# Kernel optimization log

Hardware: AMD Instinct MI355X
Metric: run time of the kernel (lower is better)

Reference implementation:

```python
import jax, jax.numpy as jnp
import numpy as np

B, S, D, H = 4, 2048, 1024, 16
DK = D // H


def setup_inputs() -> dict:
    key = jax.random.key(0)
    ks = jax.random.split(key, 12)
    inp = {
        'q': jax.random.normal(ks[0], (B, S, D), jnp.float32),
        'k': jax.random.normal(ks[1], (B, S, D), jnp.float32),
        'v': jax.random.normal(ks[2], (B, S, D), jnp.float32),
        # causal mask, broadcast over batch and heads
        'mask': jnp.tril(jnp.ones((S, S), jnp.int32))[None, None, :, :],
        'wq_w': jax.random.normal(ks[3], (D, D), jnp.float32) / np.sqrt(D),
        'wq_b': jax.random.normal(ks[4], (D,), jnp.float32) * 0.01,
        'wk_w': jax.random.normal(ks[5], (D, D), jnp.float32) / np.sqrt(D),
        'wk_b': jax.random.normal(ks[6], (D,), jnp.float32) * 0.01,
        'wv_w': jax.random.normal(ks[7], (D, D), jnp.float32) / np.sqrt(D),
        'wv_b': jax.random.normal(ks[8], (D,), jnp.float32) * 0.01,
        'wo_w': jax.random.normal(ks[9], (D, D), jnp.float32) / np.sqrt(D),
        'wo_b': jax.random.normal(ks[10], (D,), jnp.float32) * 0.01,
    }
    return inp


def reference(q, k, v, mask, wq_w, wq_b, wk_w, wk_b, wv_w, wv_b, wo_w, wo_b):
    # torch Linear: y = x @ W.T + b
    def split_heads(x):
        b, s, _ = x.shape
        return x.reshape(b, s, H, DK).transpose(0, 2, 1, 3)  # [B,H,S,DK]

    query = split_heads(q @ wq_w.T + wq_b)
    key_ = split_heads(k @ wk_w.T + wk_b)
    value = split_heads(v @ wv_w.T + wv_b)

    scores = jnp.einsum('bhqd,bhkd->bhqk', query, key_) / jnp.sqrt(
        jnp.asarray(DK, query.dtype))
    scores = jnp.where(mask == 0, jnp.asarray(-1e9, scores.dtype), scores)
    attn = jax.nn.softmax(scores, axis=-1)  # dropout=0.0 (eval)
    x = jnp.einsum('bhqk,bhkd->bhqd', attn, value)
    x = x.transpose(0, 2, 1, 3).reshape(q.shape[0], q.shape[1], D)
    out = x @ wo_w.T + wo_b
    return (out, attn)
```

## Files before the change

kernel.cpp:

```cpp
#include <hip/hip_runtime.h>
#include <stdint.h>

typedef unsigned short u16;
typedef short short8 __attribute__((ext_vector_type(8)));
typedef float f32x4 __attribute__((ext_vector_type(4)));

#define NB 4
#define NS 2048
#define ND 1024
#define NH 16
#define NDK 64

__device__ __forceinline__ u16 f2bf(float f) {
    union { float f; uint32_t i; } x; x.f = f;
    uint32_t r = x.i + 0x7FFFu + ((x.i >> 16) & 1u);
    return (u16)(r >> 16);
}
__device__ __forceinline__ float bf2f(u16 u) {
    union { uint32_t i; float f; } x; x.i = ((uint32_t)u) << 16; return x.f;
}
__device__ __forceinline__ short8 cvt8(const float* __restrict__ p) {
    float4 a = *(const float4*)p;
    float4 b = *(const float4*)(p + 4);
    short8 r;
    r[0] = (short)f2bf(a.x); r[1] = (short)f2bf(a.y);
    r[2] = (short)f2bf(a.z); r[3] = (short)f2bf(a.w);
    r[4] = (short)f2bf(b.x); r[5] = (short)f2bf(b.y);
    r[6] = (short)f2bf(b.z); r[7] = (short)f2bf(b.w);
    return r;
}

template<int MODE>
__global__ __launch_bounds__(256) void gemm128(
    const void* __restrict__ Av, const float* __restrict__ Bt,
    const float* __restrict__ bias, void* __restrict__ Cv)
{
    __shared__ __align__(16) u16 As[128 * 40];
    __shared__ __align__(16) u16 Bs[128 * 40];
    const int tid  = threadIdx.x;
    const int lane = tid & 63;
    const int w    = tid >> 6;
    const int wm   = (w >> 1) * 64;
    const int wn   = (w & 1) * 64;
    const int l15  = lane & 15;
    const int quad = lane >> 4;
    const int K    = 1024;
    int mt, nt;
    if (MODE == 2) { mt = blockIdx.x & 7; nt = blockIdx.x >> 3; }
    else           { mt = blockIdx.x >> 3; nt = blockIdx.x & 7; }
    const int m0 = mt * 128, n0 = nt * 128;

    f32x4 acc[4][4];
    const f32x4 zf = {0.f, 0.f, 0.f, 0.f};
#pragma unroll
    for (int i = 0; i < 4; ++i)
#pragma unroll
        for (int j = 0; j < 4; ++j) acc[i][j] = zf;

    const int r0 = tid >> 2;
    const int c0 = (tid & 3) * 8;

    const float* Af = (const float*)Av;
    const u16*   Ab = (const u16*)Av;
    const float* Bp = Bt + (size_t)(n0 + r0) * K + c0;

    for (int k0 = 0; k0 < K; k0 += 32) {
        __syncthreads();
        short8 a0, a1;
        if (MODE == 3) {
            a0 = *(const short8*)(Ab + (size_t)(m0 + r0) * K + c0 + k0);
            a1 = *(const short8*)(Ab + (size_t)(m0 + r0 + 64) * K + c0 + k0);
        } else {
            a0 = cvt8(Af + (size_t)(m0 + r0) * K + c0 + k0);
            a1 = cvt8(Af + (size_t)(m0 + r0 + 64) * K + c0 + k0);
        }
        short8 b0 = cvt8(Bp + k0);
        short8 b1 = cvt8(Bp + k0 + (size_t)64 * K);
        *(short8*)(As + r0 * 40 + c0)        = a0;
        *(short8*)(As + (r0 + 64) * 40 + c0) = a1;
        *(short8*)(Bs + r0 * 40 + c0)        = b0;
        *(short8*)(Bs + (r0 + 64) * 40 + c0) = b1;
        __syncthreads();
        short8 af[4], bfr[4];
#pragma unroll
        for (int i = 0; i < 4; ++i)
            af[i] = *(const short8*)(As + (wm + i * 16 + l15) * 40 + quad * 8);
#pragma unroll
        for (int j = 0; j < 4; ++j)
            bfr[j] = *(const short8*)(Bs + (wn + j * 16 + l15) * 40 + quad * 8);
#pragma unroll
        for (int i = 0; i < 4; ++i)
#pragma unroll
            for (int j = 0; j < 4; ++j)
                acc[i][j] = __builtin_amdgcn_mfma_f32_16x16x32_bf16(af[i], bfr[j], acc[i][j], 0, 0, 0);
    }

    if (MODE != 2) {
#pragma unroll
        for (int j = 0; j < 4; ++j) {
            const int n = n0 + wn + j * 16 + l15;
            const float bv = bias[n];
#pragma unroll
            for (int i = 0; i < 4; ++i) {
#pragma unroll
                for (int r = 0; r < 4; ++r) {
                    const int m = m0 + wm + i * 16 + quad * 4 + r;
                    const float vv = acc[i][j][r] + bv;
                    if (MODE == 3) {
                        ((float*)Cv)[(size_t)m * ND + n] = vv;
                    } else {
                        const size_t idx = ((size_t)((m >> 11) * NH + (n >> 6)) << 17)
                                         + (size_t)(m & (NS - 1)) * NDK + (n & (NDK - 1));
                        ((u16*)Cv)[idx] = f2bf(vv);
                    }
                }
            }
        }
    } else {
#pragma unroll
        for (int i = 0; i < 4; ++i) {
#pragma unroll
            for (int r = 0; r < 4; ++r) {
                const int m = m0 + wm + i * 16 + quad * 4 + r;
                const float bv = bias[m];
#pragma unroll
                for (int j = 0; j < 4; ++j) {
                    const int n = n0 + wn + j * 16 + l15;
                    const float vv = acc[i][j][r] + bv;
                    const size_t idx = ((size_t)((n >> 11) * NH + (m >> 6)) << 17)
                                     + (size_t)(m & (NDK - 1)) * NS + (n & (NS - 1));
                    ((u16*)Cv)[idx] = f2bf(vv);
                }
            }
        }
    }
}

__global__ __launch_bounds__(256) void attn64(
    const u16* __restrict__ Qh, const u16* __restrict__ Kh,
    const u16* __restrict__ Vt, float* __restrict__ attn,
    u16* __restrict__ X)
{
    __shared__ __align__(16) u16 Qs[64 * 72];
    __shared__ __align__(16) u16 Ks[64 * 72];
    __shared__ __align__(16) u16 Vs[64 * 72];
    __shared__ __align__(16) u16 Ps[64 * 72];
    const int tid  = threadIdx.x;
    const int lane = tid & 63;
    const int w    = tid >> 6;
    const int l15  = lane & 15;
    const int quad = lane >> 4;
    const int q0 = blockIdx.x * 64;
    const int bh = blockIdx.y;
    const u16* Qp = Qh + ((size_t)bh * NS + q0) * NDK;
    const u16* Kp = Kh + (size_t)bh * NS * NDK;
    const u16* Vp = Vt + (size_t)bh * NDK * NS;

    const int lr = tid >> 3;
    const int lc = (tid & 7) * 8;

    *(uint4*)(Qs + lr * 72 + lc)        = *(const uint4*)(Qp + (size_t)lr * NDK + lc);
    *(uint4*)(Qs + (lr + 32) * 72 + lc) = *(const uint4*)(Qp + (size_t)(lr + 32) * NDK + lc);
    __syncthreads();

    const int qrow = q0 + w * 16 + quad * 4;

    float m_r[4], l_r[4];
#pragma unroll
    for (int r = 0; r < 4; ++r) { m_r[r] = -1e30f; l_r[r] = 0.f; }

    const int nkt = (q0 >> 6) + 1;

    for (int kt = 0; kt < nkt; ++kt) {
        const int k0 = kt * 64;
        __syncthreads();
        *(uint4*)(Ks + lr * 72 + lc)        = *(const uint4*)(Kp + (size_t)(k0 + lr) * NDK + lc);
        *(uint4*)(Ks + (lr + 32) * 72 + lc) = *(const uint4*)(Kp + (size_t)(k0 + lr + 32) * NDK + lc);
        __syncthreads();

        f32x4 sa[4];
        const f32x4 zf = {0.f, 0.f, 0.f, 0.f};
#pragma unroll
        for (int j = 0; j < 4; ++j) sa[j] = zf;
#pragma unroll
        for (int ks = 0; ks < 64; ks += 32) {
            const short8 a = *(const short8*)(Qs + (w * 16 + l15) * 72 + ks + quad * 8);
#pragma unroll
            for (int j = 0; j < 4; ++j) {
                const short8 b = *(const short8*)(Ks + (j * 16 + l15) * 72 + ks + quad * 8);
                sa[j] = __builtin_amdgcn_mfma_f32_16x16x32_bf16(a, b, sa[j], 0, 0, 0);
            }
        }
        float s[4][4];
#pragma unroll
        for (int j = 0; j < 4; ++j) {
            const int kg = k0 + j * 16 + l15;
#pragma unroll
            for (int r = 0; r < 4; ++r)
                s[j][r] = (kg > qrow + r) ? -1e9f : sa[j][r] * 0.125f;
        }
#pragma unroll
        for (int r = 0; r < 4; ++r) {
            float mx = fmaxf(fmaxf(s[0][r], s[1][r]), fmaxf(s[2][r], s[3][r]));
            mx = fmaxf(mx, __shfl_xor(mx, 1));
            mx = fmaxf(mx, __shfl_xor(mx, 2));
            mx = fmaxf(mx, __shfl_xor(mx, 4));
            mx = fmaxf(mx, __shfl_xor(mx, 8));
            const float mn = fmaxf(m_r[r], mx);
            float sum = __expf(s[0][r] - mn) + __expf(s[1][r] - mn)
                      + __expf(s[2][r] - mn) + __expf(s[3][r] - mn);
            sum += __shfl_xor(sum, 1);
            sum += __shfl_xor(sum, 2);
            sum += __shfl_xor(sum, 4);
            sum += __shfl_xor(sum, 8);
            l_r[r] = l_r[r] * __expf(m_r[r] - mn) + sum;
            m_r[r] = mn;
        }
    }

    float rl[4];
#pragma unroll
    for (int r = 0; r < 4; ++r) rl[r] = 1.f / l_r[r];

    f32x4 oa[4];
    {
        const f32x4 zf = {0.f, 0.f, 0.f, 0.f};
#pragma unroll
        for (int j = 0; j < 4; ++j) oa[j] = zf;
    }

    float* arow = attn + (size_t)bh * NS * NS;

    for (int kt = 0; kt < NS / 64; ++kt) {
        const int k0 = kt * 64;
        if (k0 < q0 + 64) {
            __syncthreads();
            *(uint4*)(Ks + lr * 72 + lc)        = *(const uint4*)(Kp + (size_t)(k0 + lr) * NDK + lc);
            *(uint4*)(Ks + (lr + 32) * 72 + lc) = *(const uint4*)(Kp + (size_t)(k0 + lr + 32) * NDK + lc);
            *(uint4*)(Vs + lr * 72 + lc)        = *(const uint4*)(Vp + (size_t)lr * NS + k0 + lc);
            *(uint4*)(Vs + (lr + 32) * 72 + lc) = *(const uint4*)(Vp + (size_t)(lr + 32) * NS + k0 + lc);
            __syncthreads();

            f32x4 sa[4];
            const f32x4 zf = {0.f, 0.f, 0.f, 0.f};
#pragma unroll
            for (int j = 0; j < 4; ++j) sa[j] = zf;
#pragma unroll
            for (int ks = 0; ks < 64; ks += 32) {
                const short8 a = *(const short8*)(Qs + (w * 16 + l15) * 72 + ks + quad * 8);
#pragma unroll
                for (int j = 0; j < 4; ++j) {
                    const short8 b = *(const short8*)(Ks + (j * 16 + l15) * 72 + ks + quad * 8);
                    sa[j] = __builtin_amdgcn_mfma_f32_16x16x32_bf16(a, b, sa[j], 0, 0, 0);
                }
            }
#pragma unroll
            for (int j = 0; j < 4; ++j) {
                const int kg = k0 + j * 16 + l15;
#pragma unroll
                for (int r = 0; r < 4; ++r) {
                    float p = 0.f;
                    if (kg <= qrow + r) p = __expf(sa[j][r] * 0.125f - m_r[r]) * rl[r];
                    Ps[(w * 16 + quad * 4 + r) * 72 + j * 16 + l15] = f2bf(p);
                }
            }
            {
                const int row = lane >> 2;
                const int cc  = (lane & 3) * 16;
                const int qg  = q0 + w * 16 + row;
                const u16* ps = Ps + (w * 16 + row) * 72 + cc;
                float* dst = arow + (size_t)qg * NS + k0 + cc;
#pragma unroll
                for (int t = 0; t < 4; ++t) {
                    float4 o;
                    o.x = bf2f(ps[t * 4 + 0]);
                    o.y = bf2f(ps[t * 4 + 1]);
                    o.z = bf2f(ps[t * 4 + 2]);
                    o.w = bf2f(ps[t * 4 + 3]);
                    *(float4*)(dst + t * 4) = o;
                }
            }
#pragma unroll
            for (int ks = 0; ks < 64; ks += 32) {
                const short8 a = *(const short8*)(Ps + (w * 16 + l15) * 72 + ks + quad * 8);
#pragma unroll
                for (int j = 0; j < 4; ++j) {
                    const short8 b = *(const short8*)(Vs + (j * 16 + l15) * 72 + ks + quad * 8);
                    oa[j] = __builtin_amdgcn_mfma_f32_16x16x32_bf16(a, b, oa[j], 0, 0, 0);
                }
            }
        } else {
            const int row = lane >> 2;
            const int cc  = (lane & 3) * 16;
            const int qg  = q0 + w * 16 + row;
            float* dst = arow + (size_t)qg * NS + k0 + cc;
            const float4 z = make_float4(0.f, 0.f, 0.f, 0.f);
#pragma unroll
            for (int t = 0; t < 4; ++t) *(float4*)(dst + t * 4) = z;
        }
    }

    const int b = bh >> 4, h = bh & 15;
#pragma unroll
    for (int j = 0; j < 4; ++j) {
        const int dk = j * 16 + l15;
#pragma unroll
        for (int r = 0; r < 4; ++r) {
            const int qg = qrow + r;
            X[((size_t)b * NS + qg) * ND + (size_t)h * NDK + dk] = f2bf(oa[j][r]);
        }
    }
}

extern "C" void kernel_launch(void* const* d_in, const int* in_sizes, int n_in,
                              void* d_out, int out_size, void* d_ws, size_t ws_size,
                              hipStream_t stream) {
    const float* q    = (const float*)d_in[0];
    const float* k    = (const float*)d_in[1];
    const float* v    = (const float*)d_in[2];
    const float* wq_w = (const float*)d_in[4];
    const float* wq_b = (const float*)d_in[5];
    const float* wk_w = (const float*)d_in[6];
    const float* wk_b = (const float*)d_in[7];
    const float* wv_w = (const float*)d_in[8];
    const float* wv_b = (const float*)d_in[9];
    const float* wo_w = (const float*)d_in[10];
    const float* wo_b = (const float*)d_in[11];

    float* out  = (float*)d_out;
    float* attn = out + (size_t)NB * NS * ND;

    u16* ws = (u16*)d_ws;
    const size_t seg = (size_t)NB * NH * NS * NDK;
    u16* Qh = ws;
    u16* Kh = Qh + seg;
    u16* Vt = Kh + seg;
    u16* X  = Vt + seg;

    gemm128<0><<<dim3(512), dim3(256), 0, stream>>>((const void*)q, wq_w, wq_b, (void*)Qh);
    gemm128<0><<<dim3(512), dim3(256), 0, stream>>>((const void*)k, wk_w, wk_b, (void*)Kh);
    gemm128<2><<<dim3(512), dim3(256), 0, stream>>>((const void*)wv_w, v, wv_b, (void*)Vt);
    attn64<<<dim3(NS / 64, NB * NH), dim3(256), 0, stream>>>(Qh, Kh, Vt, attn, X);
    gemm128<3><<<dim3(512), dim3(256), 0, stream>>>((const void*)X, wo_w, wo_b, (void*)out);
}
```

Baseline: 1.656 ms.

## Load attention operands per-wave into registers, drop block syncs, reverse tile order

```diff
diff --git a/kernel.cpp b/kernel.cpp
--- a/kernel.cpp
+++ b/kernel.cpp
@@ -141,27 +141,23 @@
     const u16* __restrict__ Vt, float* __restrict__ attn,
     u16* __restrict__ X)
 {
-    __shared__ __align__(16) u16 Qs[64 * 72];
-    __shared__ __align__(16) u16 Ks[64 * 72];
-    __shared__ __align__(16) u16 Vs[64 * 72];
-    __shared__ __align__(16) u16 Ps[64 * 72];
+    __shared__ __align__(16) u16 Ps[4][16 * 72];
     const int tid  = threadIdx.x;
     const int lane = tid & 63;
     const int w    = tid >> 6;
     const int l15  = lane & 15;
     const int quad = lane >> 4;
-    const int q0 = blockIdx.x * 64;
+    const int q0 = ((int)gridDim.x - 1 - (int)blockIdx.x) * 64;
     const int bh = blockIdx.y;
     const u16* Qp = Qh + ((size_t)bh * NS + q0) * NDK;
     const u16* Kp = Kh + (size_t)bh * NS * NDK;
     const u16* Vp = Vt + (size_t)bh * NDK * NS;
-
-    const int lr = tid >> 3;
-    const int lc = (tid & 7) * 8;
-
-    *(uint4*)(Qs + lr * 72 + lc)        = *(const uint4*)(Qp + (size_t)lr * NDK + lc);
-    *(uint4*)(Qs + (lr + 32) * 72 + lc) = *(const uint4*)(Qp + (size_t)(lr + 32) * NDK + lc);
-    __syncthreads();
+    u16* Pw = &Ps[w][0];
+
+    short8 aq[2];
+#pragma unroll
+    for (int ks = 0; ks < 2; ++ks)
+        aq[ks] = *(const short8*)(Qp + (size_t)(w * 16 + l15) * NDK + ks * 32 + quad * 8);
 
     const int qrow = q0 + w * 16 + quad * 4;
 
@@ -173,31 +169,38 @@
 
     for (int kt = 0; kt < nkt; ++kt) {
         const int k0 = kt * 64;
-        __syncthreads();
-        *(uint4*)(Ks + lr * 72 + lc)        = *(const uint4*)(Kp + (size_t)(k0 + lr) * NDK + lc);
-        *(uint4*)(Ks + (lr + 32) * 72 + lc) = *(const uint4*)(Kp + (size_t)(k0 + lr + 32) * NDK + lc);
-        __syncthreads();
+        short8 bk[2][4];
+#pragma unroll
+        for (int ks = 0; ks < 2; ++ks)
+#pragma unroll
+            for (int j = 0; j < 4; ++j)
+                bk[ks][j] = *(const short8*)(Kp + (size_t)(k0 + j * 16 + l15) * NDK + ks * 32 + quad * 8);
 
         f32x4 sa[4];
         const f32x4 zf = {0.f, 0.f, 0.f, 0.f};
 #pragma unroll
         for (int j = 0; j < 4; ++j) sa[j] = zf;
 #pragma unroll
-        for (int ks = 0; ks < 64; ks += 32) {
-            const short8 a = *(const short8*)(Qs + (w * 16 + l15) * 72 + ks + quad * 8);
+        for (int ks = 0; ks < 2; ++ks)
+#pragma unroll
+            for (int j = 0; j < 4; ++j)
+                sa[j] = __builtin_amdgcn_mfma_f32_16x16x32_bf16(aq[ks], bk[ks][j], sa[j], 0, 0, 0);
+
+        float s[4][4];
+        if (kt == nkt - 1) {
 #pragma unroll
             for (int j = 0; j < 4; ++j) {
-                const short8 b = *(const short8*)(Ks + (j * 16 + l15) * 72 + ks + quad * 8);
-                sa[j] = __builtin_amdgcn_mfma_f32_16x16x32_bf16(a, b, sa[j], 0, 0, 0);
+                const int kg = k0 + j * 16 + l15;
+#pragma unroll
+                for (int r = 0; r < 4; ++r)
+                    s[j][r] = (kg > qrow + r) ? -1e9f : sa[j][r] * 0.125f;
             }
-        }
-        float s[4][4];
-#pragma unroll
-        for (int j = 0; j < 4; ++j) {
-            const int kg = k0 + j * 16 + l15;
-#pragma unroll
-            for (int r = 0; r < 4; ++r)
-                s[j][r] = (kg > qrow + r) ? -1e9f : sa[j][r] * 0.125f;
+        } else {
+#pragma unroll
+            for (int j = 0; j < 4; ++j)
+#pragma unroll
+                for (int r = 0; r < 4; ++r)
+                    s[j][r] = sa[j][r] * 0.125f;
         }
 #pragma unroll
         for (int r = 0; r < 4; ++r) {
@@ -231,70 +234,65 @@
 
     float* arow = attn + (size_t)bh * NS * NS;
 
-    for (int kt = 0; kt < NS / 64; ++kt) {
+    for (int kt = 0; kt < nkt; ++kt) {
         const int k0 = kt * 64;
-        if (k0 < q0 + 64) {
-            __syncthreads();
-            *(uint4*)(Ks + lr * 72 + lc)        = *(const uint4*)(Kp + (size_t)(k0 + lr) * NDK + lc);
-            *(uint4*)(Ks + (lr + 32) * 72 + lc) = *(const uint4*)(Kp + (size_t)(k0 + lr + 32) * NDK + lc);
-            *(uint4*)(Vs + lr * 72 + lc)        = *(const uint4*)(Vp + (size_t)lr * NS + k0 + lc);
-            *(uint4*)(Vs + (lr + 32) * 72 + lc) = *(const uint4*)(Vp + (size_t)(lr + 32) * NS + k0 + lc);
-            __syncthreads();
-
-            f32x4 sa[4];
-            const f32x4 zf = {0.f, 0.f, 0.f, 0.f};
-#pragma unroll
-            for (int j = 0; j < 4; ++j) sa[j] = zf;
-#pragma unroll
-            for (int ks = 0; ks < 64; ks += 32) {
-                const short8 a = *(const short8*)(Qs + (w * 16 + l15) * 72 + ks + quad * 8);
-#pragma unroll
-                for (int j = 0; j < 4; ++j) {
-                    const short8 b = *(const short8*)(Ks + (j * 16 + l15) * 72 + ks + quad * 8);
-                    sa[j] = __builtin_amdgcn_mfma_f32_16x16x32_bf16(a, b, sa[j], 0, 0, 0);
-                }
+        const bool diag = (kt == nkt - 1);
+
+        short8 bk[2][4];
+#pragma unroll
+        for (int ks = 0; ks < 2; ++ks)
+#pragma unroll
+            for (int j = 0; j < 4; ++j)
+                bk[ks][j] = *(const short8*)(Kp + (size_t)(k0 + j * 16 + l15) * NDK + ks * 32 + quad * 8);
+
+        f32x4 sa[4];
+        const f32x4 zf = {0.f, 0.f, 0.f, 0.f};
+#pragma unroll
+        for (int j = 0; j < 4; ++j) sa[j] = zf;
+#pragma unroll
+        for (int ks = 0; ks < 2; ++ks)
+#pragma unroll
+            for (int j = 0; j < 4; ++j)
+                sa[j] = __builtin_amdgcn_mfma_f32_16x16x32_bf16(aq[ks], bk[ks][j], sa[j], 0, 0, 0);
+
+#pragma unroll
+        for (int r = 0; r < 4; ++r) {
+            float* ar = arow + (size_t)(qrow + r) * NS + k0 + l15;
+#pragma unroll
+            for (int j = 0; j < 4; ++j) {
+                float p = __expf(sa[j][r] * 0.125f - m_r[r]) * rl[r];
+                if (diag && (k0 + j * 16 + l15 > qrow + r)) p = 0.f;
+                ar[j * 16] = p;
+                Pw[(quad * 4 + r) * 72 + j * 16 + l15] = f2bf(p);
             }
-#pragma unroll
-            for (int j = 0; j < 4; ++j) {
-                const int kg = k0 + j * 16 + l15;
-#pragma unroll
-                for (int r = 0; r < 4; ++r) {
-                    float p = 0.f;
-                    if (kg <= qrow + r) p = __expf(sa[j][r] * 0.125f - m_r[r]) * rl[r];
-                    Ps[(w * 16 + quad * 4 + r) * 72 + j * 16 + l15] = f2bf(p);
-                }
-            }
-            {
-                const int row = lane >> 2;
-                const int cc  = (lane & 3) * 16;
-                const int qg  = q0 + w * 16 + row;
-                const u16* ps = Ps + (w * 16 + row) * 72 + cc;
-                float* dst = arow + (size_t)qg * NS + k0 + cc;
-#pragma unroll
-                for (int t = 0; t < 4; ++t) {
-                    float4 o;
-                    o.x = bf2f(ps[t * 4 + 0]);
-                    o.y = bf2f(ps[t * 4 + 1]);
-                    o.z = bf2f(ps[t * 4 + 2]);
-                    o.w = bf2f(ps[t * 4 + 3]);
-                    *(float4*)(dst + t * 4) = o;
-                }
-            }
-#pragma unroll
-            for (int ks = 0; ks < 64; ks += 32) {
-                const short8 a = *(const short8*)(Ps + (w * 16 + l15) * 72 + ks + quad * 8);
-#pragma unroll
-                for (int j = 0; j < 4; ++j) {
-                    const short8 b = *(const short8*)(Vs + (j * 16 + l15) * 72 + ks + quad * 8);
-                    oa[j] = __builtin_amdgcn_mfma_f32_16x16x32_bf16(a, b, oa[j], 0, 0, 0);
-                }
-            }
-        } else {
-            const int row = lane >> 2;
-            const int cc  = (lane & 3) * 16;
-            const int qg  = q0 + w * 16 + row;
-            float* dst = arow + (size_t)qg * NS + k0 + cc;
-            const float4 z = make_float4(0.f, 0.f, 0.f, 0.f);
+        }
+
+        short8 bv[2][4];
+#pragma unroll
+        for (int ks = 0; ks < 2; ++ks)
+#pragma unroll
+            for (int j = 0; j < 4; ++j)
+                bv[ks][j] = *(const short8*)(Vp + (size_t)(j * 16 + l15) * NS + k0 + ks * 32 + quad * 8);
+
+        short8 pa[2];
+#pragma unroll
+        for (int ks = 0; ks < 2; ++ks)
+            pa[ks] = *(const short8*)(Pw + l15 * 72 + ks * 32 + quad * 8);
+
+#pragma unroll
+        for (int ks = 0; ks < 2; ++ks)
+#pragma unroll
+            for (int j = 0; j < 4; ++j)
+                oa[j] = __builtin_amdgcn_mfma_f32_16x16x32_bf16(pa[ks], bv[ks][j], oa[j], 0, 0, 0);
+    }
+
+    {
+        const int row = lane >> 2;
+        const int cc  = (lane & 3) * 16;
+        const int qg  = q0 + w * 16 + row;
+        const float4 z = make_float4(0.f, 0.f, 0.f, 0.f);
+        for (int kt = nkt; kt < NS / 64; ++kt) {
+            float* dst = arow + (size_t)qg * NS + kt * 64 + cc;
 #pragma unroll
             for (int t = 0; t < 4; ++t) *(float4*)(dst + t * 4) = z;
         }
```

Result: slower. 2.221 ms (+34.2%).
